# Performance work log

Hardware: AMD Instinct MI355X
Metric: run time of the kernel (lower is better)

## Reference

```python
import jax, jax.numpy as jnp
import numpy as np

B = 1024
IN = 512      # in_features
O = 64        # out_features
E = 8         # ensamble
K = O * E     # total tiny MLPs, index k = i*E + j (i: output, j: ensemble)


def setup_inputs() -> dict:
    key = jax.random.key(0)
    k1, k2, k3, k4, k5 = jax.random.split(key, 5)
    s = 1.0 / np.sqrt(IN)
    X = jax.random.normal(k1, (B, IN), dtype=jnp.float32)
    # Stacked weights for all K = O*E tiny MLPs.
    # nn.Linear(in,in): y = x @ W1^T + b1, W1: [in_out, in_in]
    W1 = jax.random.uniform(k2, (K, IN, IN), jnp.float32, -s, s)
    b1 = jax.random.uniform(k3, (K, IN), jnp.float32, -s, s)
    # nn.Linear(in,1): W2 squeezed to [K, IN], b2 to [K]
    W2 = jax.random.uniform(k4, (K, IN), jnp.float32, -s, s)
    b2 = jax.random.uniform(k5, (K,), jnp.float32, -s, s)
    return {"X": X, "W1": W1, "b1": b1, "W2": W2, "b2": b2}


def reference(X, W1, b1, W2, b2):
    # h[b,k,:] = relu(X[b] @ W1[k].T + b1[k])  -- one batched GEMM
    h = jax.nn.relu(jnp.einsum('bi,kji->bkj', X, W1) + b1)  # [B,K,IN]
    out = jnp.einsum('bkj,kj->bk', h, W2) + b2              # [B,K]
    # original: concat over ensemble (dim=-1) then stack over out_features (dim=-1)
    out = out.reshape(X.shape[0], O, E).transpose(0, 2, 1)  # [B,E,O]
    return out
```

## Files before the change

kernel.cpp:

```cpp
#include <hip/hip_runtime.h>
#include <hip/hip_bf16.h>

typedef __attribute__((ext_vector_type(8))) short short8;
typedef __attribute__((ext_vector_type(4))) float f32x4;

__device__ __forceinline__ short8 pack8(const f32x4& a, const f32x4& b) {
    union { __hip_bfloat162 h[4]; short8 s; } u;
    u.h[0] = __float22bfloat162_rn(make_float2(a[0], a[1]));
    u.h[1] = __float22bfloat162_rn(make_float2(a[2], a[3]));
    u.h[2] = __float22bfloat162_rn(make_float2(b[0], b[1]));
    u.h[3] = __float22bfloat162_rn(make_float2(b[2], b[3]));
    return u.s;
}

__device__ __forceinline__ int swz4(int g) { return g ^ (((g >> 4) & 3) << 1); }

__global__ __launch_bounds__(256)
void ens_cvt(const float* __restrict__ X, const float* __restrict__ W1,
             short* __restrict__ WS)
{
    const int t = threadIdx.x, lane = t & 63, wv = t >> 6;
    const int g = blockIdx.x * 4 + wv;
    const int row16 = lane & 15, koct = lane >> 4;
    const float* src;
    short* dst;
    if (blockIdx.x < 4096) {
        const int km = g >> 5, f = g & 31;
        src = W1 + (size_t)km * 262144 + (size_t)(f * 16 + row16) * 512 + koct * 8;
        dst = WS + (size_t)km * 262144 + (size_t)(f * 16) * 512 + lane * 8;
    } else {
        const int mf = g - 16384;
        src = X + (size_t)(mf * 16 + row16) * 512 + koct * 8;
        dst = WS + 134217728ull + (size_t)(mf * 16) * 512 + lane * 8;
    }
#pragma unroll
    for (int ks = 0; ks < 16; ++ks) {
        f32x4 a = *(const f32x4*)(src + ks * 32);
        f32x4 b = *(const f32x4*)(src + ks * 32 + 4);
        *(short8*)(dst + ks * 512) = pack8(a, b);
    }
}

#define LOADSET(AV, BV, POFF)                                                 \
  do {                                                                        \
    _Pragma("unroll") for (int mi = 0; mi < 8; ++mi)                          \
        AV[mi] = *(const short8*)(pa + mi * 8192 + (POFF));                   \
    _Pragma("unroll") for (int pp = 0; pp < 4; ++pp)                          \
        BV[pp] = *(const short8*)(pb + pp * 8192 + (POFF));                   \
  } while (0)

#define MM(AV, BV)                                                            \
  do {                                                                        \
    __builtin_amdgcn_s_setprio(1);                                            \
    _Pragma("unroll") for (int mi = 0; mi < 8; ++mi)                          \
        _Pragma("unroll") for (int pp = 0; pp < 4; ++pp)                      \
            acc[mi][pp] = __builtin_amdgcn_mfma_f32_16x16x32_bf16(            \
                AV[mi], BV[pp], acc[mi][pp], 0, 0, 0);                        \
    __builtin_amdgcn_s_setprio(0);                                            \
  } while (0)

__global__ __launch_bounds__(512, 2)
void ens_gemm_direct(const short* __restrict__ Xb, const short* __restrict__ W1b,
                     const float* __restrict__ B1, const float* __restrict__ W2,
                     const float* __restrict__ B2, float* __restrict__ out)
{
    __shared__ float lout[1024];
    const int t    = threadIdx.x;
    const int lane = t & 63;
    const int wv   = t >> 6;
    const int wm   = wv >> 2;
    const int wn   = wv & 3;

    const int bb  = blockIdx.x;
    const int xcd = bb & 7;
    const int j   = bb >> 3;
    const int km  = xcd * 64 + (j >> 3);
    const int sub = j & 7;
    const int mt  = sub >> 1;
    const int nt  = sub & 1;

    const short* pa = Xb + (size_t)(mt * 16 + wm * 8) * 8192 + lane * 8;
    const short* pb = W1b + (size_t)km * 262144 +
                      (size_t)(nt * 16 + wn * 4) * 8192 + lane * 8;

    f32x4 acc[8][4];
#pragma unroll
    for (int i = 0; i < 8; ++i)
#pragma unroll
        for (int p = 0; p < 4; ++p)
            acc[i][p] = (f32x4)0.0f;

    short8 avP[8], bvP[4], avQ[8], bvQ[4];

    LOADSET(avP, bvP, 0);
    LOADSET(avQ, bvQ, 512);
    pa += 1024; pb += 1024;

#pragma unroll 1
    for (int kt = 0; kt < 7; ++kt) {
        MM(avP, bvP);
        LOADSET(avP, bvP, 0);
        MM(avQ, bvQ);
        LOADSET(avQ, bvQ, 512);
        pa += 1024; pb += 1024;
    }
    MM(avP, bvP);
    MM(avQ, bvQ);

    const int nc = lane & 15;
    const int kq = lane >> 4;
    float b1v[4], w2v[4];
#pragma unroll
    for (int pp = 0; pp < 4; ++pp) {
        int n = nt * 256 + (wn * 4 + pp) * 16 + nc;
        b1v[pp] = B1[km * 512 + n];
        w2v[pp] = W2[km * 512 + n];
    }

#pragma unroll
    for (int i = 0; i < 8; ++i) {
#pragma unroll
        for (int r = 0; r < 4; ++r) {
            float s = 0.f;
#pragma unroll
            for (int pp = 0; pp < 4; ++pp) {
                float h = acc[i][pp][r] + b1v[pp];
                h = h > 0.f ? h : 0.f;
                s += h * w2v[pp];
            }
#pragma unroll
            for (int d = 1; d < 16; d <<= 1)
                s += __shfl_xor(s, d, 64);
            if (nc == 0) {
                int row = wm * 128 + i * 16 + kq * 4 + r;
                lout[row * 4 + wn] = s;
            }
        }
    }
    __syncthreads();
    if (t < 256) {
        float s = lout[t * 4 + 0] + lout[t * 4 + 1] + lout[t * 4 + 2] + lout[t * 4 + 3];
        if (nt == 0) s += B2[km];
        int b = mt * 256 + t;
        atomicAdd(out + (size_t)b * 512 + (km & 7) * 64 + (km >> 3), s);
    }
}

#define FISSUE(S, BASE, KT1)                                                  \
  do {                                                                        \
    const float* q_ = (BASE) + (KT1) * 64;                                    \
    S[0] = *(const f32x4*)q_;          S[1] = *(const f32x4*)(q_ + 4);        \
    S[2] = *(const f32x4*)(q_ + 32);   S[3] = *(const f32x4*)(q_ + 36);       \
    const float* q2_ = q_ + 65536;                                            \
    S[4] = *(const f32x4*)q2_;         S[5] = *(const f32x4*)(q2_ + 4);       \
    S[6] = *(const f32x4*)(q2_ + 32);  S[7] = *(const f32x4*)(q2_ + 36);      \
  } while (0)

#define FWRITEB(S, WB, OPOFF)                                                 \
  do {                                                                        \
    char* d0_ = (WB) + (OPOFF) + wfrag;                                       \
    *(short8*)d0_ = pack8(S[0], S[1]);                                        \
    *(short8*)(d0_ + 1024) = pack8(S[2], S[3]);                               \
    char* d1_ = d0_ + 16384;                                                  \
    *(short8*)d1_ = pack8(S[4], S[5]);                                        \
    *(short8*)(d1_ + 1024) = pack8(S[6], S[7]);                               \
  } while (0)

#define FKK(RB, KKV)                                                          \
  do {                                                                        \
    _Pragma("unroll") for (int mi = 0; mi < 8; ++mi)                          \
        av[mi] = *(const short8*)((RB) +                                      \
            (((wm * 8 + mi) * 2 + (KKV)) << 10) + rdo);                       \
    _Pragma("unroll") for (int pp = 0; pp < 4; ++pp)                          \
        bv[pp] = *(const short8*)((RB) + 32768 +                              \
            (((wn * 4 + pp) * 2 + (KKV)) << 10) + rdo);                       \
    __builtin_amdgcn_s_setprio(1);                                            \
    _Pragma("unroll") for (int mi = 0; mi < 8; ++mi)                          \
        _Pragma("unroll") for (int pp = 0; pp < 4; ++pp)                      \
            acc[mi][pp] = __builtin_amdgcn_mfma_f32_16x16x32_bf16(            \
                av[mi], bv[pp], acc[mi][pp], 0, 0, 0);                        \
    __builtin_amdgcn_s_setprio(0);                                            \
  } while (0)

#define FPRO_WRITE(TT, ROFF)                                                  \
  do {                                                                        \
    short8 a_ = pack8(TT[0], TT[1]);                                          \
    short8 b_ = pack8(TT[2], TT[3]);                                          \
    char* d_ = smem + (ROFF) + wfrag;                                         \
    *(short8*)d_ = a_;                                                        \
    *(short8*)(d_ + 1024) = b_;                                               \
  } while (0)

__global__ __launch_bounds__(512, 2)
void ens_mlp_fallback(const float* __restrict__ X,
                      const float* __restrict__ W1,
                      const float* __restrict__ B1,
                      const float* __restrict__ W2,
                      const float* __restrict__ B2,
                      float* __restrict__ out)
{
    extern __shared__ char smem[];
    const int t    = threadIdx.x;
    const int lane = t & 63;
    const int wv   = t >> 6;
    const int wm   = wv >> 2;
    const int wn   = wv & 3;

    const int bb  = blockIdx.x;
    const int xcd = bb & 7;
    const int j   = bb >> 3;
    const int km  = xcd * 64 + (j >> 3);
    const int sub = j & 7;
    const int mt  = sub >> 1;
    const int nt  = sub & 1;

    const float* __restrict__ W1k = W1 + (size_t)km * (512 * 512);

    const int lr = t >> 2;
    const int c  = t & 3;
    const float* As = X   + (size_t)(mt * 256 + lr) * 512 + c * 8;
    const float* Bs = W1k + (size_t)(nt * 256 + lr) * 512 + c * 8;
    const int wfrag = ((lr >> 4) << 11) + (swz4((c << 4) | (lr & 15)) << 4);
    const int rdo   = swz4(lane) << 4;

    {
        f32x4 t0[4], t1[4], t2[4], t3[4];
        const float* q;
        q = As;          t0[0]=*(const f32x4*)q; t0[1]=*(const f32x4*)(q+4); t0[2]=*(const f32x4*)(q+32); t0[3]=*(const f32x4*)(q+36);
        q = As + 65536;  t1[0]=*(const f32x4*)q; t1[1]=*(const f32x4*)(q+4); t1[2]=*(const f32x4*)(q+32); t1[3]=*(const f32x4*)(q+36);
        q = Bs;          t2[0]=*(const f32x4*)q; t2[1]=*(const f32x4*)(q+4); t2[2]=*(const f32x4*)(q+32); t2[3]=*(const f32x4*)(q+36);
        q = Bs + 65536;  t3[0]=*(const f32x4*)q; t3[1]=*(const f32x4*)(q+4); t3[2]=*(const f32x4*)(q+32); t3[3]=*(const f32x4*)(q+36);
        asm volatile("s_waitcnt vmcnt(12)" ::: "memory"); FPRO_WRITE(t0, 0);
        asm volatile("s_waitcnt vmcnt(8)"  ::: "memory"); FPRO_WRITE(t1, 16384);
        asm volatile("s_waitcnt vmcnt(4)"  ::: "memory"); FPRO_WRITE(t2, 32768);
        asm volatile("s_waitcnt vmcnt(0)"  ::: "memory"); FPRO_WRITE(t3, 49152);
        asm volatile("s_waitcnt lgkmcnt(0)" ::: "memory");
        __builtin_amdgcn_sched_barrier(0);
        __builtin_amdgcn_s_barrier();
    }

    f32x4 acc[8][4];
#pragma unroll
    for (int i = 0; i < 8; ++i)
#pragma unroll
        for (int p = 0; p < 4; ++p)
            acc[i][p] = (f32x4)0.0f;

    short8 av[8], bv[4];
    f32x4 sS[8];

#pragma unroll 1
    for (int kt = 0; kt < 7; ++kt) {
        const char* rb = smem + (kt & 1) * 65536;
        char* wb       = smem + ((kt + 1) & 1) * 65536;

        FISSUE(sS, Bs, kt + 1);
        FKK(rb, 0);
        asm volatile("s_waitcnt vmcnt(0)" ::: "memory");
        FWRITEB(sS, wb, 32768);
        FISSUE(sS, As, kt + 1);
        FKK(rb, 1);
        asm volatile("s_waitcnt vmcnt(0)" ::: "memory");
        FWRITEB(sS, wb, 0);
        asm volatile("s_waitcnt lgkmcnt(0)" ::: "memory");
        __builtin_amdgcn_sched_barrier(0);
        __builtin_amdgcn_s_barrier();
    }
    {
        const char* rb = smem + 65536;
        FKK(rb, 0);
        FKK(rb, 1);
    }

    const int nc = lane & 15;
    const int kq = lane >> 4;
    float b1v[4], w2v[4];
#pragma unroll
    for (int pp = 0; pp < 4; ++pp) {
        int n = nt * 256 + (wn * 4 + pp) * 16 + nc;
        b1v[pp] = B1[km * 512 + n];
        w2v[pp] = W2[km * 512 + n];
    }

    float* lout = (float*)smem;
#pragma unroll
    for (int i = 0; i < 8; ++i) {
#pragma unroll
        for (int r = 0; r < 4; ++r) {
            float s = 0.f;
#pragma unroll
            for (int pp = 0; pp < 4; ++pp) {
                float h = acc[i][pp][r] + b1v[pp];
                h = h > 0.f ? h : 0.f;
                s += h * w2v[pp];
            }
#pragma unroll
            for (int d = 1; d < 16; d <<= 1)
                s += __shfl_xor(s, d, 64);
            if (nc == 0) {
                int row = wm * 128 + i * 16 + kq * 4 + r;
                lout[row * 4 + wn] = s;
            }
        }
    }
    __syncthreads();
    if (t < 256) {
        float s = lout[t * 4 + 0] + lout[t * 4 + 1] + lout[t * 4 + 2] + lout[t * 4 + 3];
        if (nt == 0) s += B2[km];
        int b = mt * 256 + t;
        atomicAdd(out + (size_t)b * 512 + (km & 7) * 64 + (km >> 3), s);
    }
}

extern "C" void kernel_launch(void* const* d_in, const int* in_sizes, int n_in,
                              void* d_out, int out_size, void* d_ws, size_t ws_size,
                              hipStream_t stream) {
    const float* X  = (const float*)d_in[0];
    const float* W1 = (const float*)d_in[1];
    const float* B1 = (const float*)d_in[2];
    const float* W2 = (const float*)d_in[3];
    const float* B2 = (const float*)d_in[4];
    float* out = (float*)d_out;

    hipMemsetAsync(out, 0, (size_t)out_size * sizeof(float), stream);

    const size_t NEED = 269484032ull;
    if (ws_size >= NEED) {
        short* WS = (short*)d_ws;
        ens_cvt<<<dim3(4112), dim3(256), 0, stream>>>(X, W1, WS);
        ens_gemm_direct<<<dim3(4096), dim3(512), 0, stream>>>(
            WS + 134217728ull, WS, B1, W2, B2, out);
    } else {
        ens_mlp_fallback<<<dim3(4096), dim3(512), 131072, stream>>>(
            X, W1, B1, W2, B2, out);
    }
}
```

Before: 519.6 us.

## Stage GEMM operands through double-buffered LDS via global_load_lds DMA

Replaces direct per-wave global loads of the A and B fragments with global_load_lds transfers into a double-buffered 128KB LDS area. Each wave now loads a distinct slice instead of waves redundantly loading shared A/B tiles. MFMAs are interleaved with LDS reads under manual waitcnt and sched_barrier control. The goal is to cut redundant global/L2 traffic and overlap copies with compute. The cost is 128KB of LDS per block, which limits occupancy to one block per CU and defeats the launch_bounds(512,2) hint, plus a barrier every k-step.

New measurement: 473.8 us. 1.1x faster.

```diff
diff --git a/kernel.cpp b/kernel.cpp
--- a/kernel.cpp
+++ b/kernel.cpp
@@ -14,6 +14,11 @@
 }
 
 __device__ __forceinline__ int swz4(int g) { return g ^ (((g >> 4) & 3) << 1); }
+
+#define GLDS(GP, LP)                                                          \
+    __builtin_amdgcn_global_load_lds(                                         \
+        (__attribute__((address_space(1))) void*)(void*)(GP),                 \
+        (__attribute__((address_space(3))) void*)(void*)(LP), 16, 0, 0)
 
 __global__ __launch_bounds__(256)
 void ens_cvt(const float* __restrict__ X, const float* __restrict__ W1,
@@ -41,32 +46,47 @@
     }
 }
 
-#define LOADSET(AV, BV, POFF)                                                 \
-  do {                                                                        \
-    _Pragma("unroll") for (int mi = 0; mi < 8; ++mi)                          \
-        AV[mi] = *(const short8*)(pa + mi * 8192 + (POFF));                   \
+#define SB __builtin_amdgcn_sched_barrier(0)
+
+#define RDA4(DST, MI0, KKV)                                                   \
+    _Pragma("unroll") for (int ii = 0; ii < 4; ++ii)                          \
+        DST[ii] = *(const short8*)(rb +                                       \
+            (((wm * 8 + (MI0) + ii) * 2 + (KKV)) << 10) + l16);
+
+#define RDB4(DST, KKV)                                                        \
     _Pragma("unroll") for (int pp = 0; pp < 4; ++pp)                          \
-        BV[pp] = *(const short8*)(pb + pp * 8192 + (POFF));                   \
-  } while (0)
-
-#define MM(AV, BV)                                                            \
-  do {                                                                        \
+        DST[pp] = *(const short8*)(rb + 32768 +                               \
+            (((wn * 4 + pp) * 2 + (KKV)) << 10) + l16);
+
+#define MFMA16(AV, BV, AOFF)                                                  \
     __builtin_amdgcn_s_setprio(1);                                            \
-    _Pragma("unroll") for (int mi = 0; mi < 8; ++mi)                          \
+    _Pragma("unroll") for (int ii = 0; ii < 4; ++ii)                          \
         _Pragma("unroll") for (int pp = 0; pp < 4; ++pp)                      \
-            acc[mi][pp] = __builtin_amdgcn_mfma_f32_16x16x32_bf16(            \
-                AV[mi], BV[pp], acc[mi][pp], 0, 0, 0);                        \
-    __builtin_amdgcn_s_setprio(0);                                            \
-  } while (0)
+            acc[(AOFF) + ii][pp] = __builtin_amdgcn_mfma_f32_16x16x32_bf16(   \
+                AV[ii], BV[pp], acc[(AOFF) + ii][pp], 0, 0, 0);               \
+    __builtin_amdgcn_s_setprio(0);
+
+#define GLDS4A(KOFF)                                                          \
+    GLDS(gsrc + (KOFF) + 0,     wdst + 0);                                    \
+    GLDS(gsrc + (KOFF) + 512,   wdst + 1024);                                 \
+    GLDS(gsrc + (KOFF) + 8192,  wdst + 2048);                                 \
+    GLDS(gsrc + (KOFF) + 8704,  wdst + 3072);
+
+#define GLDS4B(KOFF)                                                          \
+    GLDS(gsrc + (KOFF) + 16384, wdst + 4096);                                 \
+    GLDS(gsrc + (KOFF) + 16896, wdst + 5120);                                 \
+    GLDS(gsrc + (KOFF) + 24576, wdst + 6144);                                 \
+    GLDS(gsrc + (KOFF) + 25088, wdst + 7168);
 
 __global__ __launch_bounds__(512, 2)
-void ens_gemm_direct(const short* __restrict__ Xb, const short* __restrict__ W1b,
-                     const float* __restrict__ B1, const float* __restrict__ W2,
-                     const float* __restrict__ B2, float* __restrict__ out)
+void ens_gemm_dma(const short* __restrict__ Xb, const short* __restrict__ W1b,
+                  const float* __restrict__ B1, const float* __restrict__ W2,
+                  const float* __restrict__ B2, float* __restrict__ out)
 {
-    __shared__ float lout[1024];
+    extern __shared__ char smem[];
     const int t    = threadIdx.x;
     const int lane = t & 63;
+    const int l16  = lane << 4;
     const int wv   = t >> 6;
     const int wm   = wv >> 2;
     const int wn   = wv & 3;
@@ -79,9 +99,16 @@
     const int mt  = sub >> 1;
     const int nt  = sub & 1;
 
-    const short* pa = Xb + (size_t)(mt * 16 + wm * 8) * 8192 + lane * 8;
-    const short* pb = W1b + (size_t)km * 262144 +
-                      (size_t)(nt * 16 + wn * 4) * 8192 + lane * 8;
+    const short* gsrc;
+    int wvoff;
+    if (wv < 4) {
+        gsrc  = Xb + (size_t)(mt * 16 + wv * 4) * 8192 + lane * 8;
+        wvoff = wv * 8192;
+    } else {
+        gsrc  = W1b + (size_t)km * 262144 +
+                (size_t)(nt * 16 + (wv - 4) * 4) * 8192 + lane * 8;
+        wvoff = 32768 + (wv - 4) * 8192;
+    }
 
     f32x4 acc[8][4];
 #pragma unroll
@@ -90,22 +117,59 @@
         for (int p = 0; p < 4; ++p)
             acc[i][p] = (f32x4)0.0f;
 
-    short8 avP[8], bvP[4], avQ[8], bvQ[4];
-
-    LOADSET(avP, bvP, 0);
-    LOADSET(avQ, bvQ, 512);
-    pa += 1024; pb += 1024;
+    short8 avP[4], avQ[4], avR[4];
+    short8 bvP[4], bvQ[4];
+
+    {
+        char* wdst = smem + wvoff;
+        GLDS4A(0);
+        GLDS4B(0);
+        asm volatile("s_waitcnt vmcnt(0)" ::: "memory");
+        SB;
+        __builtin_amdgcn_s_barrier();
+    }
 
 #pragma unroll 1
-    for (int kt = 0; kt < 7; ++kt) {
-        MM(avP, bvP);
-        LOADSET(avP, bvP, 0);
-        MM(avQ, bvQ);
-        LOADSET(avQ, bvQ, 512);
-        pa += 1024; pb += 1024;
-    }
-    MM(avP, bvP);
-    MM(avQ, bvQ);
+    for (int kt = 0; kt < 8; ++kt) {
+        const char* rb = smem + (kt & 1) * 65536;
+        char* wdst     = smem + ((kt + 1) & 1) * 65536 + wvoff;
+        const int koff = (kt + 1) << 10;
+        const bool stage = (kt < 7);
+
+        RDA4(avP, 0, 0);
+        RDB4(bvP, 0);
+        SB;
+        RDA4(avQ, 4, 0);
+        SB;
+        if (stage) { GLDS4A(koff); }
+        asm volatile("s_waitcnt lgkmcnt(4)" ::: "memory");
+        SB;
+        MFMA16(avP, bvP, 0);
+        SB;
+
+        RDA4(avR, 0, 1);
+        RDB4(bvQ, 1);
+        SB;
+        if (stage) { GLDS4B(koff); }
+        asm volatile("s_waitcnt lgkmcnt(8)" ::: "memory");
+        SB;
+        MFMA16(avQ, bvP, 4);
+        SB;
+
+        RDA4(avP, 4, 1);
+        SB;
+        asm volatile("s_waitcnt lgkmcnt(4)" ::: "memory");
+        SB;
+        MFMA16(avR, bvQ, 0);
+        SB;
+
+        asm volatile("s_waitcnt lgkmcnt(0)" ::: "memory");
+        if (stage) { asm volatile("s_waitcnt vmcnt(0)" ::: "memory"); }
+        SB;
+        MFMA16(avP, bvQ, 4);
+        SB;
+        __builtin_amdgcn_s_barrier();
+    }
 
     const int nc = lane & 15;
     const int kq = lane >> 4;
@@ -117,6 +181,7 @@
         w2v[pp] = W2[km * 512 + n];
     }
 
+    float* lout = (float*)smem;
 #pragma unroll
     for (int i = 0; i < 8; ++i) {
 #pragma unroll
@@ -328,7 +393,7 @@
     if (ws_size >= NEED) {
         short* WS = (short*)d_ws;
         ens_cvt<<<dim3(4112), dim3(256), 0, stream>>>(X, W1, WS);
-        ens_gemm_direct<<<dim3(4096), dim3(512), 0, stream>>>(
+        ens_gemm_dma<<<dim3(4096), dim3(512), 131072, stream>>>(
             WS + 134217728ull, WS, B1, W2, B2, out);
     } else {
         ens_mlp_fallback<<<dim3(4096), dim3(512), 131072, stream>>>(
```
